# Kernel optimization log

Measured on AMD Instinct MI355X. Metric: run time of the kernel, lower is better.

## Reference

```python
import jax, jax.numpy as jnp
import numpy as np

VOC, MEM, NSLOTS, NSENT, MAXLEN, QLEN, ANSLEN, B = 32000, 128, 20, 128, 32, 16, 8, 64


def _xavier(k, shape):
    fan_out, fan_in = shape
    std = jnp.sqrt(2.0 / (fan_in + fan_out))
    return (jax.random.normal(k, shape, jnp.float32) * std).astype(jnp.float32)


def setup_inputs() -> dict:
    key = jax.random.key(0)
    ks = jax.random.split(key, 12)
    inp = {}
    inp["input_ids"] = jax.random.randint(ks[0], (B, NSENT, MAXLEN), 0, VOC)
    inp["question"] = jax.random.randint(ks[1], (B, QLEN), 0, VOC)
    inp["ans"] = jax.random.randint(ks[2], (B, ANSLEN, 2), 0, VOC)
    E = jax.random.normal(ks[3], (VOC, MEM), jnp.float32)
    inp["E"] = E.at[0].set(0.0)  # padding_idx=0
    inp["Uw"] = _xavier(ks[4], (MEM, MEM)); inp["Ub"] = jnp.zeros((MEM,), jnp.float32)
    inp["Vw"] = _xavier(ks[5], (MEM, MEM)); inp["Vb"] = jnp.zeros((MEM,), jnp.float32)
    inp["Ww"] = _xavier(ks[6], (MEM, MEM)); inp["Wb"] = jnp.zeros((MEM,), jnp.float32)
    inp["slot_keys"] = jax.random.normal(ks[7], (NSLOTS, MEM), jnp.float32)  # self.w
    inp["Hw"] = _xavier(ks[8], (MEM, MEM)); inp["Hb"] = jnp.zeros((MEM,), jnp.float32)
    return inp


def reference(input_ids, question, ans, E, Uw, Ub, Vw, Vb, Ww, Wb, slot_keys, Hw, Hb):
    E0 = E.at[0].set(0.0)  # padding row stays zero
    bsz = input_ids.shape[0]
    n_sent = input_ids.shape[1]
    tok = input_ids.reshape(bsz, -1)
    # original indexes s[:, t, :] for t < n_sent over the flattened story
    s = E0[tok[:, :n_sent]]                       # [B, T, m]
    Ws = jnp.einsum('btm,nm->btn', s, Ww) + Wb    # precompute W(s_t): [B, T, m]
    Vkey = slot_keys @ Vw.T + Vb                  # [J, m]

    def step(mem, xs):
        # mem: [B, J, m]
        s_t, ws_t = xs                            # [B, m], [B, m]
        g = jax.nn.sigmoid(jnp.einsum('bm,bjm->bj', s_t, mem) + s_t @ slot_keys.T)  # [B, J]
        h_cand = jax.nn.relu(
            jnp.einsum('bjm,nm->bjn', mem, Uw) + Ub
            + Vkey[None, :, :] + ws_t[:, None, :]
        )  # dropout is identity in eval mode
        mem = mem + g[..., None] * h_cand
        # torch.norm(mem_j): global Frobenius norm over (batch, mem) per slot
        norms = jnp.sqrt(jnp.sum(mem * mem, axis=(0, 2), keepdims=True))
        return mem / norms, None

    mem0 = jnp.zeros((bsz, slot_keys.shape[0], s.shape[-1]), s.dtype)
    h, _ = jax.lax.scan(step, mem0, (jnp.swapaxes(s, 0, 1), jnp.swapaxes(Ws, 0, 1)))
    # output module
    q = E0[question].mean(1)                      # [B, m]
    a1 = E0[ans[:, :, 0]].mean(1)                 # [B, m]
    a2 = E0[ans[:, :, 1]].mean(1)                 # [B, m]
    p = jax.nn.softmax(jnp.einsum('bjm,bm->bj', h, q), axis=-1)   # [B, J]
    u = jnp.einsum('bj,bjm->bm', p, h)            # [B, m]
    r = jax.nn.relu(q + u @ Hw.T + Hb)            # [B, m]
    y1 = jnp.sum(r * a1, axis=1)
    y2 = jnp.sum(r * a2, axis=1)
    return jax.nn.softmax(jnp.stack((y1, y2), axis=1), axis=1)
```

## Files before the change

### kernel.cpp

```cpp
#include <hip/hip_runtime.h>
#include <math.h>


typedef __attribute__((ext_vector_type(8)))  short bf16x8;
typedef __attribute__((ext_vector_type(16))) float f32x16;

__device__ __forceinline__ unsigned short f2bh(float x) {
    unsigned int u = __float_as_uint(x);
    u += 0x7FFFu + ((u >> 16) & 1u);
    return (unsigned short)(u >> 16);
}
__device__ __forceinline__ float blo(unsigned int w) { return __uint_as_float(w << 16); }
__device__ __forceinline__ float bhi(unsigned int w) { return __uint_as_float(w & 0xFFFF0000u); }

template<int CTRL>
__device__ __forceinline__ float dpp_add0(float x) {
    int y = __builtin_amdgcn_update_dpp(0, __float_as_int(x), CTRL, 0xF, 0xF, true);
    return x + __int_as_float(y);
}

#define LDS_BARRIER() do {                                   \
    asm volatile("s_waitcnt lgkmcnt(0)" ::: "memory");       \
    __builtin_amdgcn_s_barrier();                            \
    asm volatile("" ::: "memory");                           \
} while (0)

__global__ __launch_bounds__(128) void prep_kernel(
    const int* __restrict__ ids, const int* __restrict__ ques, const int* __restrict__ ans,
    const float* __restrict__ E, const float* __restrict__ Ww, const float* __restrict__ Wb,
    const float* __restrict__ Vw, const float* __restrict__ Vb, const float* __restrict__ skeys,
    float* __restrict__ sT, float* __restrict__ WsT, float* __restrict__ vkey,
    float* __restrict__ qv, float* __restrict__ a1v, float* __restrict__ a2v,
    float* __restrict__ SK)
{
    const int bi  = blockIdx.x;
    const int tid = threadIdx.x;
    __shared__ float s_l[8][132];
    __shared__ float sk_l[20 * 132];
    __shared__ float k_l[128];
    if (bi < 1024) {
        const int b = bi >> 4;
        const int g = bi & 15;
        for (int r = tid; r < 2560; r += 128) sk_l[(r >> 7) * 132 + (r & 127)] = skeys[r];
        for (int tt = 0; tt < 8; ++tt) {
            const int t     = g * 8 + tt;
            const int token = ids[b * 4096 + t];
            const float v   = E[token * 128 + tid];
            s_l[tt][tid] = v;
            sT[(t * 64 + b) * 128 + tid] = v;
        }
        __syncthreads();
        float acc[8];
        const float wbn = Wb[tid];
        #pragma unroll
        for (int i = 0; i < 8; ++i) acc[i] = wbn;
        const float4* wrow = (const float4*)(Ww + tid * 128);
        for (int m4 = 0; m4 < 32; ++m4) {
            const float4 w = wrow[m4];
            #pragma unroll
            for (int tt = 0; tt < 8; ++tt) {
                acc[tt] += s_l[tt][m4*4+0]*w.x + s_l[tt][m4*4+1]*w.y
                         + s_l[tt][m4*4+2]*w.z + s_l[tt][m4*4+3]*w.w;
            }
        }
        for (int tt = 0; tt < 8; ++tt)
            WsT[((g*8+tt) * 64 + b) * 128 + tid] = acc[tt];
        for (int idx = tid; idx < 160; idx += 128) {
            const int tt = idx / 20;
            const int jj = idx - tt * 20;
            float d = 0.f;
            for (int m = 0; m < 128; ++m) d += s_l[tt][m] * sk_l[jj * 132 + m];
            SK[(jj * 128 + (g*8 + tt)) * 64 + b] = d;
        }
    } else if (bi < 1044) {
        const int j = bi - 1024;
        k_l[tid] = skeys[j * 128 + tid];
        __syncthreads();
        float acc = Vb[tid];
        const float4* vrow = (const float4*)(Vw + tid * 128);
        for (int m4 = 0; m4 < 32; ++m4) {
            const float4 w = vrow[m4];
            acc += k_l[m4*4]*w.x + k_l[m4*4+1]*w.y + k_l[m4*4+2]*w.z + k_l[m4*4+3]*w.w;
        }
        vkey[j * 128 + tid] = acc;
    } else {
        const int b = bi - 1044;
        float sq = 0.f, s1 = 0.f, s2 = 0.f;
        for (int i = 0; i < 16; ++i) sq += E[ques[b*16+i] * 128 + tid];
        for (int i = 0; i < 8;  ++i) s1 += E[ans[(b*8+i)*2+0] * 128 + tid];
        for (int i = 0; i < 8;  ++i) s2 += E[ans[(b*8+i)*2+1] * 128 + tid];
        qv [b*128+tid] = sq * (1.f/16.f);
        a1v[b*128+tid] = s1 * 0.125f;
        a2v[b*128+tid] = s2 * 0.125f;
    }
}

__global__ __launch_bounds__(512, 1) void scan_kernel(
    const float* __restrict__ sT, const float* __restrict__ WsT,
    const float* __restrict__ vkey, const float* __restrict__ Uw,
    const float* __restrict__ Ub, const float* __restrict__ SK,
    float* __restrict__ h_out)
{
    __shared__ unsigned short AB[64 * 136];
    __shared__ float g_l[64];
    __shared__ float wred[8];

    const int j    = blockIdx.x;
    const int tid  = threadIdx.x;
    const int wave = tid >> 6;
    const int lane = tid & 63;
    const int l32  = lane & 31;
    const int q    = lane >> 5;
    const int bt2  = wave & 1;
    const int nt2  = wave >> 1;
    const int n    = nt2 * 32 + l32;
    const int gb   = tid >> 3;
    const int gm   = (tid & 7) * 16;

    bf16x8 b_h[8];
    {
        const int k0 = q * 8;
        #pragma unroll
        for (int kc = 0; kc < 8; ++kc) {
            const float4* src = (const float4*)(Uw + n * 128 + kc * 16 + k0);
            const float4 v0 = src[0], v1 = src[1];
            const float xs[8] = {v0.x,v0.y,v0.z,v0.w, v1.x,v1.y,v1.z,v1.w};
            #pragma unroll
            for (int e = 0; e < 8; ++e) b_h[kc][e] = (short)f2bh(xs[e]);
        }
    }
    for (int i = tid; i < 64 * 136 / 2; i += 512) ((unsigned int*)AB)[i] = 0u;
    const float ubv = Ub[n] + vkey[j * 128 + n];

    unsigned woffB[16];
    #pragma unroll
    for (int r = 0; r < 16; ++r) {
        const int brow = bt2*32 + 4*q + (r & 3) + 8*(r >> 2);
        woffB[r] = (unsigned)((brow * 128 + n) * 4);
    }
    const unsigned soffB = (unsigned)((gb * 128 + gm) * 4);
    const unsigned koffB = (unsigned)(gb * 4);
    const char* SKj = (const char*)SK + (size_t)j * 32768;

    float xprev[16];
    #pragma unroll
    for (int r = 0; r < 16; ++r) xprev[r] = 0.f;

    float4 svA0, svA1, svA2, svA3, svB0, svB1, svB2, svB3;
    float  skvA, skvB;
    float  wsv[16];
    {
        const float4* s4 = (const float4*)((const char*)sT + soffB);
        svA0 = s4[0]; svA1 = s4[1]; svA2 = s4[2]; svA3 = s4[3];
        skvA = *(const float*)(SKj + koffB);
        const char* pW = (const char*)WsT;
        #pragma unroll
        for (int r = 0; r < 16; ++r) wsv[r] = *(const float*)(pW + woffB[r]);
    }
    __syncthreads();

    float inv_s = 1.f;

#define SCAN_STEP(T_CUR, Sc0,Sc1,Sc2,Sc3,SKc, Sn0,Sn1,Sn2,Sn3,SKn)             \
    {                                                                          \
        const int tn = (T_CUR < 127) ? (T_CUR) + 1 : 127;                      \
                        \
        {                                                                      \
            const float4* s4 = (const float4*)((const char*)sT + (size_t)tn * 32768 + soffB); \
            Sn0 = s4[0]; Sn1 = s4[1]; Sn2 = s4[2]; Sn3 = s4[3];                \
            SKn = *(const float*)(SKj + (size_t)tn * 256 + koffB);             \
        }                                                                      \
               \
        {                                                                      \
            const uint4* u4 = (const uint4*)(AB + gb * 136 + gm);              \
            const uint4 w0 = u4[0], w1 = u4[1];                                \
            float a0 = Sc0.x*blo(w0.x), a1 = Sc0.y*bhi(w0.x);                  \
            float a2 = Sc0.z*blo(w0.y), a3 = Sc0.w*bhi(w0.y);                  \
            a0 = fmaf(Sc1.x, blo(w0.z), a0); a1 = fmaf(Sc1.y, bhi(w0.z), a1);  \
            a2 = fmaf(Sc1.z, blo(w0.w), a2); a3 = fmaf(Sc1.w, bhi(w0.w), a3);  \
            a0 = fmaf(Sc2.x, blo(w1.x), a0); a1 = fmaf(Sc2.y, bhi(w1.x), a1);  \
            a2 = fmaf(Sc2.z, blo(w1.y), a2); a3 = fmaf(Sc2.w, bhi(w1.y), a3);  \
            a0 = fmaf(Sc3.x, blo(w1.z), a0); a1 = fmaf(Sc3.y, bhi(w1.z), a1);  \
            a2 = fmaf(Sc3.z, blo(w1.w), a2); a3 = fmaf(Sc3.w, bhi(w1.w), a3);  \
            float d1 = (a0 + a1) + (a2 + a3);                                  \
            d1 = dpp_add0<0x111>(d1);                           \
            d1 = dpp_add0<0x112>(d1);                           \
            d1 = dpp_add0<0x114>(d1);   \
            if ((tid & 7) == 7) {                                              \
                const float e = __expf(-(inv_s * d1 + SKc));                   \
                g_l[gb] = __builtin_amdgcn_rcpf(1.f + e);                      \
            }                                                                  \
        }                                                                      \
                         \
        f32x16 acc0 = {0.f,0.f,0.f,0.f,0.f,0.f,0.f,0.f,                        \
                       0.f,0.f,0.f,0.f,0.f,0.f,0.f,0.f};                       \
        f32x16 acc1 = acc0;                                                    \
        {                                                                      \
            const unsigned short* arow = AB + (bt2*32 + l32) * 136 + q * 8;    \
            _Pragma("unroll")                                                  \
            for (int kc = 0; kc < 8; ++kc) {                                   \
                const bf16x8 a = *(const bf16x8*)(arow + kc * 16);             \
                if (kc & 1) acc1 = __builtin_amdgcn_mfma_f32_32x32x16_bf16(a, b_h[kc], acc1, 0, 0, 0); \
                else        acc0 = __builtin_amdgcn_mfma_f32_32x32x16_bf16(a, b_h[kc], acc0, 0, 0, 0); \
            }                                                                  \
            acc0 += acc1;      \
        }                                                                      \
        LDS_BARRIER();                 \
                                    \
        const float4 gA = *(const float4*)(g_l + bt2*32 + 4*q + 0);            \
        const float4 gB = *(const float4*)(g_l + bt2*32 + 4*q + 8);            \
        const float4 gC = *(const float4*)(g_l + bt2*32 + 4*q + 16);           \
        const float4 gD = *(const float4*)(g_l + bt2*32 + 4*q + 24);           \
        const float gr[16] = {gA.x,gA.y,gA.z,gA.w, gB.x,gB.y,gB.z,gB.w,        \
                              gC.x,gC.y,gC.z,gC.w, gD.x,gD.y,gD.z,gD.w};       \
        float sq0 = 0.f, sq1 = 0.f;                                            \
        _Pragma("unroll")                                                      \
        for (int r = 0; r < 16; ++r) {                                         \
            const int brow = bt2*32 + 4*q + (r & 3) + 8*(r >> 2);              \
            float hr = fmaf(inv_s, acc0[r], ubv + wsv[r]);                     \
            hr = fmaxf(hr, 0.f);                                   \
            const float x = fmaf(inv_s, xprev[r], gr[r] * hr);                 \
            xprev[r] = x;                                 \
            AB[brow*136 + n] = (unsigned short)(__float_as_uint(x) >> 16);     \
            if (r & 1) sq1 = fmaf(x, x, sq1); else sq0 = fmaf(x, x, sq0);      \
        }                                                                      \
            \
        {                                                                      \
            const char* pW = (const char*)WsT + (size_t)tn * 32768;            \
            _Pragma("unroll")                                                  \
            for (int r = 0; r < 16; ++r)                                       \
                wsv[r] = *(const float*)(pW + woffB[r]);                       \
        }                                                                      \
                 \
        float ssq = sq0 + sq1;                                                 \
        ssq = dpp_add0<0x111>(ssq);                             \
        ssq = dpp_add0<0x112>(ssq);                             \
        ssq = dpp_add0<0x114>(ssq);                             \
        ssq = dpp_add0<0x118>(ssq);       \
        ssq = dpp_add0<0x142>(ssq);     \
        ssq = dpp_add0<0x143>(ssq);          \
        if (lane == 63) wred[wave] = ssq;                                      \
        LDS_BARRIER();     \
        const float4 w0 = *(const float4*)(wred);                              \
        const float4 w1 = *(const float4*)(wred + 4);                          \
        inv_s = __builtin_amdgcn_rsqf(w0.x+w0.y+w0.z+w0.w + w1.x+w1.y+w1.z+w1.w); \
    }

    for (int t = 0; t < 128; t += 2) {
        SCAN_STEP(t,     svA0,svA1,svA2,svA3,skvA, svB0,svB1,svB2,svB3,skvB)
        SCAN_STEP(t + 1, svB0,svB1,svB2,svB3,skvB, svA0,svA1,svA2,svA3,skvA)
    }
#undef SCAN_STEP

    #pragma unroll
    for (int r = 0; r < 16; ++r) {
        const int brow = bt2*32 + 4*q + (r & 3) + 8*(r >> 2);
        h_out[(brow*20 + j)*128 + n] = inv_s * xprev[r];
    }
}

__global__ __launch_bounds__(128) void final_kernel(
    const float* __restrict__ h, const float* __restrict__ qv,
    const float* __restrict__ a1v, const float* __restrict__ a2v,
    const float* __restrict__ Hw, const float* __restrict__ Hb,
    float* __restrict__ out)
{
    const int b   = blockIdx.x;
    const int tid = threadIdx.x;
    __shared__ float hb[20][128];
    __shared__ float ql[128];
    __shared__ float ul[128];
    __shared__ float pl[20];
    __shared__ float lgt[20];
    __shared__ float red1[2], red2[2];

    for (int jj = 0; jj < 20; ++jj) hb[jj][tid] = h[(b*20+jj)*128 + tid];
    ql[tid] = qv[b*128 + tid];
    __syncthreads();
    if (tid < 20) {
        float d = 0.f;
        for (int m = 0; m < 128; ++m) d += hb[tid][m] * ql[m];
        lgt[tid] = d;
    }
    __syncthreads();
    if (tid == 0) {
        float mx = lgt[0];
        for (int jj = 1; jj < 20; ++jj) mx = fmaxf(mx, lgt[jj]);
        float s = 0.f;
        for (int jj = 0; jj < 20; ++jj) { const float e = expf(lgt[jj]-mx); pl[jj] = e; s += e; }
        const float is = 1.f / s;
        for (int jj = 0; jj < 20; ++jj) pl[jj] *= is;
    }
    __syncthreads();
    float u = 0.f;
    for (int jj = 0; jj < 20; ++jj) u += pl[jj] * hb[jj][tid];
    ul[tid] = u;
    __syncthreads();
    float acc = ql[tid] + Hb[tid];
    const float4* hwr = (const float4*)(Hw + tid*128);
    for (int m4 = 0; m4 < 32; ++m4) {
        const float4 w = hwr[m4];
        acc += ul[m4*4]*w.x + ul[m4*4+1]*w.y + ul[m4*4+2]*w.z + ul[m4*4+3]*w.w;
    }
    const float r  = fmaxf(acc, 0.f);
    float y1 = r * a1v[b*128+tid];
    float y2 = r * a2v[b*128+tid];
    #pragma unroll
    for (int mask = 1; mask < 64; mask <<= 1) {
        y1 += __shfl_xor(y1, mask, 64);
        y2 += __shfl_xor(y2, mask, 64);
    }
    if ((tid & 63) == 0) { red1[tid>>6] = y1; red2[tid>>6] = y2; }
    __syncthreads();
    if (tid == 0) {
        const float z1 = red1[0] + red1[1];
        const float z2 = red2[0] + red2[1];
        const float mx = fmaxf(z1, z2);
        const float e1 = expf(z1-mx), e2 = expf(z2-mx);
        const float s  = e1 + e2;
        out[b*2+0] = e1 / s;
        out[b*2+1] = e2 / s;
    }
}

extern "C" void kernel_launch(void* const* d_in, const int* in_sizes, int n_in,
                              void* d_out, int out_size, void* d_ws, size_t ws_size,
                              hipStream_t stream)
{
    const int*   ids  = (const int*)  d_in[0];
    const int*   ques = (const int*)  d_in[1];
    const int*   ans  = (const int*)  d_in[2];
    const float* E    = (const float*)d_in[3];
    const float* Uw   = (const float*)d_in[4];
    const float* Ubv  = (const float*)d_in[5];
    const float* Vw   = (const float*)d_in[6];
    const float* Vb   = (const float*)d_in[7];
    const float* Ww   = (const float*)d_in[8];
    const float* Wb   = (const float*)d_in[9];
    const float* sk   = (const float*)d_in[10];
    const float* Hw   = (const float*)d_in[11];
    const float* Hb   = (const float*)d_in[12];

    float* ws   = (float*)d_ws;
    float* sT   = ws;
    float* WsT  = sT  + 1048576;
    float* vkey = WsT + 1048576;
    float* qv   = vkey + 2560;
    float* a1v  = qv  + 8192;
    float* a2v  = a1v + 8192;
    float* h    = a2v + 8192;
    float* SK   = h   + 163840;

    prep_kernel<<<1108, 128, 0, stream>>>(ids, ques, ans, E, Ww, Wb, Vw, Vb, sk,
                                          sT, WsT, vkey, qv, a1v, a2v, SK);
    scan_kernel<<<20, 512, 0, stream>>>(sT, WsT, vkey, Uw, Ubv, SK, h);
    final_kernel<<<64, 128, 0, stream>>>(h, qv, a1v, a2v, Hw, Hb, (float*)d_out);
}
```

Before: 274.6 us.

## Store story embeddings as bf16 and use dot2 bf16 for gate dot products

The sequence embeddings sT are now written as bf16 in prep and read as packed bf16 in the scan, halving that per-step global load. The gate dot product uses the fdot2 bf16 instruction instead of unpacking and FMAs. Memory writeback to LDS is repacked via DPP lane swaps into 32-bit stores of two bf16 values instead of 16 scalar short stores. The cost is an extra rounding of s_t to bf16 and some cross-lane shuffles.

```diff
diff --git a/kernel.cpp b/kernel.cpp
--- a/kernel.cpp
+++ b/kernel.cpp
@@ -10,13 +10,32 @@
     u += 0x7FFFu + ((u >> 16) & 1u);
     return (unsigned short)(u >> 16);
 }
+__device__ __forceinline__ unsigned int packtr(float lo, float hi) {
+    return (__float_as_uint(lo) >> 16) | (__float_as_uint(hi) & 0xFFFF0000u);
+}
 __device__ __forceinline__ float blo(unsigned int w) { return __uint_as_float(w << 16); }
 __device__ __forceinline__ float bhi(unsigned int w) { return __uint_as_float(w & 0xFFFF0000u); }
+
+#if __has_builtin(__builtin_amdgcn_fdot2_f32_bf16)
+typedef __attribute__((ext_vector_type(2))) __bf16 bf16x2v;
+__device__ __forceinline__ float dot2bf(unsigned int a, unsigned int b, float c) {
+    return __builtin_amdgcn_fdot2_f32_bf16(
+        __builtin_bit_cast(bf16x2v, a), __builtin_bit_cast(bf16x2v, b), c, false);
+}
+#else
+__device__ __forceinline__ float dot2bf(unsigned int a, unsigned int b, float c) {
+    return fmaf(bhi(a), bhi(b), fmaf(blo(a), blo(b), c));
+}
+#endif
 
 template<int CTRL>
 __device__ __forceinline__ float dpp_add0(float x) {
     int y = __builtin_amdgcn_update_dpp(0, __float_as_int(x), CTRL, 0xF, 0xF, true);
     return x + __int_as_float(y);
+}
+__device__ __forceinline__ float dpp_xor1_move(float x) {
+    int y = __builtin_amdgcn_update_dpp(0, __float_as_int(x), 0xB1, 0xF, 0xF, true);
+    return __int_as_float(y);
 }
 
 #define LDS_BARRIER() do {                                   \
@@ -29,7 +48,7 @@
     const int* __restrict__ ids, const int* __restrict__ ques, const int* __restrict__ ans,
     const float* __restrict__ E, const float* __restrict__ Ww, const float* __restrict__ Wb,
     const float* __restrict__ Vw, const float* __restrict__ Vb, const float* __restrict__ skeys,
-    float* __restrict__ sT, float* __restrict__ WsT, float* __restrict__ vkey,
+    unsigned short* __restrict__ sT2, float* __restrict__ WsT, float* __restrict__ vkey,
     float* __restrict__ qv, float* __restrict__ a1v, float* __restrict__ a2v,
     float* __restrict__ SK)
 {
@@ -47,7 +66,7 @@
             const int token = ids[b * 4096 + t];
             const float v   = E[token * 128 + tid];
             s_l[tt][tid] = v;
-            sT[(t * 64 + b) * 128 + tid] = v;
+            sT2[(t * 64 + b) * 128 + tid] = f2bh(v);
         }
         __syncthreads();
         float acc[8];
@@ -96,7 +115,7 @@
 }
 
 __global__ __launch_bounds__(512, 1) void scan_kernel(
-    const float* __restrict__ sT, const float* __restrict__ WsT,
+    const unsigned short* __restrict__ sT2, const float* __restrict__ WsT,
     const float* __restrict__ vkey, const float* __restrict__ Uw,
     const float* __restrict__ Ub, const float* __restrict__ SK,
     float* __restrict__ h_out)
@@ -116,6 +135,7 @@
     const int n    = nt2 * 32 + l32;
     const int gb   = tid >> 3;
     const int gm   = (tid & 7) * 16;
+    const bool evenl = ((l32 & 1) == 0);
 
     bf16x8 b_h[8];
     {
@@ -138,20 +158,22 @@
         const int brow = bt2*32 + 4*q + (r & 3) + 8*(r >> 2);
         woffB[r] = (unsigned)((brow * 128 + n) * 4);
     }
-    const unsigned soffB = (unsigned)((gb * 128 + gm) * 4);
+    const unsigned soffB = (unsigned)((gb * 128 + gm) * 2);
     const unsigned koffB = (unsigned)(gb * 4);
     const char* SKj = (const char*)SK + (size_t)j * 32768;
+    unsigned* const wdst = (unsigned*)((char*)AB
+        + (bt2*32 + 4*q + ((l32 & 1) << 4)) * 272 + ((n & ~1) * 2));
 
     float xprev[16];
     #pragma unroll
     for (int r = 0; r < 16; ++r) xprev[r] = 0.f;
 
-    float4 svA0, svA1, svA2, svA3, svB0, svB1, svB2, svB3;
-    float  skvA, skvB;
-    float  wsv[16];
+    uint4 svA0, svA1, svB0, svB1;
+    float skvA, skvB;
+    float wsv[16];
     {
-        const float4* s4 = (const float4*)((const char*)sT + soffB);
-        svA0 = s4[0]; svA1 = s4[1]; svA2 = s4[2]; svA3 = s4[3];
+        const char* pS = (const char*)sT2 + soffB;
+        svA0 = *(const uint4*)(pS); svA1 = *(const uint4*)(pS + 16);
         skvA = *(const float*)(SKj + koffB);
         const char* pW = (const char*)WsT;
         #pragma unroll
@@ -161,33 +183,33 @@
 
     float inv_s = 1.f;
 
-#define SCAN_STEP(T_CUR, Sc0,Sc1,Sc2,Sc3,SKc, Sn0,Sn1,Sn2,Sn3,SKn)             \
+#define SCAN_STEP(T_CUR, Sc0,Sc1,SKc, Sn0,Sn1,SKn)                             \
     {                                                                          \
         const int tn = (T_CUR < 127) ? (T_CUR) + 1 : 127;                      \
                         \
         {                                                                      \
-            const float4* s4 = (const float4*)((const char*)sT + (size_t)tn * 32768 + soffB); \
-            Sn0 = s4[0]; Sn1 = s4[1]; Sn2 = s4[2]; Sn3 = s4[3];                \
+            const char* pS = (const char*)sT2 + (size_t)tn * 16384 + soffB;    \
+            Sn0 = *(const uint4*)(pS); Sn1 = *(const uint4*)(pS + 16);         \
             SKn = *(const float*)(SKj + (size_t)tn * 256 + koffB);             \
         }                                                                      \
                \
         {                                                                      \
             const uint4* u4 = (const uint4*)(AB + gb * 136 + gm);              \
             const uint4 w0 = u4[0], w1 = u4[1];                                \
-            float a0 = Sc0.x*blo(w0.x), a1 = Sc0.y*bhi(w0.x);                  \
-            float a2 = Sc0.z*blo(w0.y), a3 = Sc0.w*bhi(w0.y);                  \
-            a0 = fmaf(Sc1.x, blo(w0.z), a0); a1 = fmaf(Sc1.y, bhi(w0.z), a1);  \
-            a2 = fmaf(Sc1.z, blo(w0.w), a2); a3 = fmaf(Sc1.w, bhi(w0.w), a3);  \
-            a0 = fmaf(Sc2.x, blo(w1.x), a0); a1 = fmaf(Sc2.y, bhi(w1.x), a1);  \
-            a2 = fmaf(Sc2.z, blo(w1.y), a2); a3 = fmaf(Sc2.w, bhi(w1.y), a3);  \
-            a0 = fmaf(Sc3.x, blo(w1.z), a0); a1 = fmaf(Sc3.y, bhi(w1.z), a1);  \
-            a2 = fmaf(Sc3.z, blo(w1.w), a2); a3 = fmaf(Sc3.w, bhi(w1.w), a3);  \
-            float d1 = (a0 + a1) + (a2 + a3);                                  \
-            d1 = dpp_add0<0x111>(d1);                           \
-            d1 = dpp_add0<0x112>(d1);                           \
-            d1 = dpp_add0<0x114>(d1);   \
+            float d0 = dot2bf(w0.x, Sc0.x, 0.f);                               \
+            float d1 = dot2bf(w0.y, Sc0.y, 0.f);                               \
+            float d2 = dot2bf(w0.z, Sc0.z, 0.f);                               \
+            float d3 = dot2bf(w0.w, Sc0.w, 0.f);                               \
+            d0 = dot2bf(w1.x, Sc1.x, d0);                                      \
+            d1 = dot2bf(w1.y, Sc1.y, d1);                                      \
+            d2 = dot2bf(w1.z, Sc1.z, d2);                                      \
+            d3 = dot2bf(w1.w, Sc1.w, d3);                                      \
+            float dg = (d0 + d1) + (d2 + d3);                                  \
+            dg = dpp_add0<0x111>(dg);                           \
+            dg = dpp_add0<0x112>(dg);                           \
+            dg = dpp_add0<0x114>(dg);          \
             if ((tid & 7) == 7) {                                              \
-                const float e = __expf(-(inv_s * d1 + SKc));                   \
+                const float e = __expf(-(inv_s * dg + SKc));                   \
                 g_l[gb] = __builtin_amdgcn_rcpf(1.f + e);                      \
             }                                                                  \
         }                                                                      \
@@ -213,16 +235,26 @@
         const float4 gD = *(const float4*)(g_l + bt2*32 + 4*q + 24);           \
         const float gr[16] = {gA.x,gA.y,gA.z,gA.w, gB.x,gB.y,gB.z,gB.w,        \
                               gC.x,gC.y,gC.z,gC.w, gD.x,gD.y,gD.z,gD.w};       \
+        float xv[16];                                                          \
         float sq0 = 0.f, sq1 = 0.f;                                            \
         _Pragma("unroll")                                                      \
         for (int r = 0; r < 16; ++r) {                                         \
-            const int brow = bt2*32 + 4*q + (r & 3) + 8*(r >> 2);              \
             float hr = fmaf(inv_s, acc0[r], ubv + wsv[r]);                     \
             hr = fmaxf(hr, 0.f);                                   \
             const float x = fmaf(inv_s, xprev[r], gr[r] * hr);                 \
-            xprev[r] = x;                                 \
-            AB[brow*136 + n] = (unsigned short)(__float_as_uint(x) >> 16);     \
+            xprev[r] = x; xv[r] = x;                      \
             if (r & 1) sq1 = fmaf(x, x, sq1); else sq0 = fmaf(x, x, sq0);      \
+        }                                                                      \
+               \
+        _Pragma("unroll")                                                      \
+        for (int i = 0; i < 8; ++i) {                                          \
+            const float xa = xv[i];                                            \
+            const float xb = xv[i + 8];                                        \
+            const float sa = dpp_xor1_move(xa);                                \
+            const float sb = dpp_xor1_move(xb);                                \
+            const float lo = evenl ? xa : sb;                                  \
+            const float hi = evenl ? sa : xb;                                  \
+            wdst[((i & 3) + 8 * (i >> 2)) * 68] = packtr(lo, hi);              \
         }                                                                      \
             \
         {                                                                      \
@@ -247,8 +279,8 @@
     }
 
     for (int t = 0; t < 128; t += 2) {
-        SCAN_STEP(t,     svA0,svA1,svA2,svA3,skvA, svB0,svB1,svB2,svB3,skvB)
-        SCAN_STEP(t + 1, svB0,svB1,svB2,svB3,skvB, svA0,svA1,svA2,svA3,skvA)
+        SCAN_STEP(t,     svA0,svA1,skvA, svB0,svB1,skvB)
+        SCAN_STEP(t + 1, svB0,svB1,skvB, svA0,svA1,skvA)
     }
 #undef SCAN_STEP
 
@@ -342,17 +374,17 @@
     const float* Hb   = (const float*)d_in[12];
 
     float* ws   = (float*)d_ws;
-    float* sT   = ws;
-    float* WsT  = sT  + 1048576;
-    float* vkey = WsT + 1048576;
-    float* qv   = vkey + 2560;
-    float* a1v  = qv  + 8192;
-    float* a2v  = a1v + 8192;
-    float* h    = a2v + 8192;
-    float* SK   = h   + 163840;
+    unsigned short* sT2 = (unsigned short*)ws;
+    float* WsT  = ws    + 524288;
+    float* vkey = WsT   + 1048576;
+    float* qv   = vkey  + 2560;
+    float* a1v  = qv    + 8192;
+    float* a2v  = a1v   + 8192;
+    float* h    = a2v   + 8192;
+    float* SK   = h     + 163840;
 
     prep_kernel<<<1108, 128, 0, stream>>>(ids, ques, ans, E, Ww, Wb, Vw, Vb, sk,
-                                          sT, WsT, vkey, qv, a1v, a2v, SK);
-    scan_kernel<<<20, 512, 0, stream>>>(sT, WsT, vkey, Uw, Ubv, SK, h);
+                                          sT2, WsT, vkey, qv, a1v, a2v, SK);
+    scan_kernel<<<20, 512, 0, stream>>>(sT2, WsT, vkey, Uw, Ubv, SK, h);
     final_kernel<<<64, 128, 0, stream>>>(h, qv, a1v, a2v, Hw, Hb, (float*)d_out);
 }
```

Result: faster. 262.8 us (-4.3%).
